# Performance work log

Measured on AMD Instinct MI355X. Metric: run time of the kernel, lower is better.

The kernel has to match this reference:

```python
import jax, jax.numpy as jnp
import numpy as np

N = 100000   # nodes
E = 1600000  # edges
D_IN = 128
D = 128
G = 64       # graphs in batch
C = 2        # out_channels
EPS = 1e-5   # BatchNorm eps


def setup_inputs() -> dict:
    key = jax.random.key(0)
    ks = jax.random.split(key, 24)
    s = 0.05
    inp = {
        "x": jax.random.normal(ks[0], (N, D_IN), dtype=jnp.float32),
        "edge_index": jax.random.randint(ks[1], (2, E), 0, N, dtype=jnp.int32),
        "edge_attr": jax.random.uniform(ks[2], (E, 2), dtype=jnp.float32),
        "batch": jnp.sort(jax.random.randint(ks[3], (N,), 0, G, dtype=jnp.int32)),
        # GCN layer 0
        "Wg0": jax.random.normal(ks[4], (D_IN, D), dtype=jnp.float32) * s,
        "bg0": jnp.zeros((D,), jnp.float32),
        "gamma0": jnp.ones((D,), jnp.float32),
        "beta0": jnp.zeros((D,), jnp.float32),
        # GCN layer 1
        "Wg1": jax.random.normal(ks[5], (D, D), dtype=jnp.float32) * s,
        "bg1": jnp.zeros((D,), jnp.float32),
        "gamma1": jnp.ones((D,), jnp.float32),
        "beta1": jnp.zeros((D,), jnp.float32),
        # dense head
        "Wl1": jax.random.normal(ks[6], (D, D), dtype=jnp.float32) * s,
        "bl1": jnp.zeros((D,), jnp.float32),
        "Wl2": jax.random.normal(ks[7], (D, D), dtype=jnp.float32) * s,
        "bl2": jnp.zeros((D,), jnp.float32),
        "Wc1": jax.random.normal(ks[8], (D, D), dtype=jnp.float32) * s,
        "bc1": jnp.zeros((D,), jnp.float32),
        "Wc2": jax.random.normal(ks[9], (D, C), dtype=jnp.float32) * s,
        "bc2": jnp.zeros((C,), jnp.float32),
    }
    return inp


def _gcn_conv(x, src, dst, w, W, b):
    # PyG GCNConv: h = x @ W ; add self-loops (weight 1) ; symmetric norm ; agg at dst ; + bias
    h = x @ W                                                   # [N, D]
    deg = jax.ops.segment_sum(w, dst, num_segments=N) + 1.0     # self-loop weight 1
    dinv = jnp.where(deg > 0, jax.lax.rsqrt(deg), 0.0)          # deg^{-1/2}
    norm = dinv[src] * w * dinv[dst]                            # [E]
    agg = jax.ops.segment_sum(norm[:, None] * h[src], dst, num_segments=N)
    agg = agg + (dinv * dinv)[:, None] * h                      # self-loop contribution
    return agg + b


def _bn(x, gamma, beta):
    # training-mode batch statistics over the node dimension
    m = x.mean(axis=0)
    v = x.var(axis=0)
    return (x - m) * jax.lax.rsqrt(v + EPS) * gamma + beta


def reference(x, edge_index, edge_attr, batch,
              Wg0, bg0, gamma0, beta0,
              Wg1, bg1, gamma1, beta1,
              Wl1, bl1, Wl2, bl2, Wc1, bc1, Wc2, bc2):
    src, dst = edge_index[0], edge_index[1]
    w = edge_attr[:, 1]  # which_edge_weight is None -> column 1

    h = jax.nn.relu(_gcn_conv(x, src, dst, w, Wg0, bg0))
    h = _bn(h, gamma0, beta0)                 # dropout: identity (eval)
    h = jax.nn.relu(_gcn_conv(h, src, dst, w, Wg1, bg1))
    h = _bn(h, gamma1, beta1)

    h = jax.nn.relu(h @ Wl1 + bl1)
    h = h @ Wl2 + bl2                          # node embeddings [N, D]

    counts = jax.ops.segment_sum(jnp.ones((N,), h.dtype), batch, num_segments=G)
    graph_reps = jax.ops.segment_sum(h, batch, num_segments=G) / jnp.maximum(counts, 1.0)[:, None]

    logits = jax.nn.relu(graph_reps @ Wc1 + bc1) @ Wc2 + bc2   # [G, C]
    return (h, graph_reps, logits)
```

## Files before the change

kernel.cpp:

```cpp
#include <hip/hip_runtime.h>

#define N_NODES 100000
#define N_EDGES 1600000
#define DFEAT   128
#define NGRAPH  64
#define EPSV    1e-5f
#define SCAN_BLOCKS ((N_NODES + 255) / 256)
#define DEG_SCALE 268435456.0f
#define DEG_MASK  ((1ULL << 42) - 1)
#define EDGE_BLOCKS ((N_EDGES + 511) / 512)
#define GEMM_GRID   ((N_NODES + 127) / 128)
#define MAXDEG 64
#define DEGSTRIDE 16

typedef float v4f  __attribute__((ext_vector_type(4)));
typedef short v8s  __attribute__((ext_vector_type(8)));
typedef unsigned short us4 __attribute__((ext_vector_type(4)));
typedef unsigned short us8 __attribute__((ext_vector_type(8)));

static __device__ __forceinline__ unsigned short f2bf(float f) {
    union { float f; unsigned int u; } v; v.f = f;
    unsigned int u = v.u;
    return (unsigned short)((u + 0x7FFFu + ((u >> 16) & 1u)) >> 16);
}
static __device__ __forceinline__ float bf2f(unsigned short b) {
    union { unsigned int u; float f; } v; v.u = ((unsigned int)b) << 16;
    return v.f;
}

__global__ __launch_bounds__(256) void initprep_kernel(
    unsigned long long* __restrict__ degcnt,
    float* __restrict__ stats0, float* __restrict__ stats1,
    float* __restrict__ gsum, float* __restrict__ gcntf,
    const float* __restrict__ W0, const float* __restrict__ W1,
    const float* __restrict__ W2, const float* __restrict__ W3,
    unsigned short* __restrict__ T0, unsigned short* __restrict__ T1,
    unsigned short* __restrict__ T2, unsigned short* __restrict__ T3) {
    int bid = blockIdx.x;
    int i = bid * 256 + threadIdx.x;
    if (i < N_NODES) degcnt[(size_t)i * DEGSTRIDE] = 0ULL;
    if (i < 256)  { stats0[i] = 0.f; stats1[i] = 0.f; }
    if (i < NGRAPH * DFEAT) gsum[i] = 0.f;
    if (i < NGRAPH) gcntf[i] = 0.f;
    if (bid < 256) {
        int which = bid >> 6;
        int i2 = (bid & 63) * 256 + threadIdx.x;
        const float* W = which == 0 ? W0 : which == 1 ? W1 : which == 2 ? W2 : W3;
        unsigned short* T = which == 0 ? T0 : which == 1 ? T1 : which == 2 ? T2 : T3;
        int n = i2 >> 7, k = i2 & 127;
        T[n * 128 + k] = f2bf(W[k * 128 + n]);
    }
}

__global__ __launch_bounds__(256, 4) void edgeplace_gemm0_kernel(
    const int* __restrict__ ei, const float* __restrict__ ea,
    unsigned long long* __restrict__ degcnt, int2* __restrict__ edges2,
    const float* __restrict__ X, const unsigned short* __restrict__ Wt,
    unsigned short* __restrict__ Out) {
    __shared__ unsigned short Ws[128][136];
    if (blockIdx.x < EDGE_BLOCKS) {
        int e0 = blockIdx.x * 512 + threadIdx.x;
        int e1 = e0 + 256;
        int sA = 0, dA = 0; float wA = 0.f; bool vA = e0 < N_EDGES;
        if (vA) { sA = ei[e0]; dA = ei[N_EDGES + e0]; wA = ea[2 * e0 + 1]; }
        int sB = 0, dB = 0; float wB = 0.f; bool vB = e1 < N_EDGES;
        if (vB) { sB = ei[e1]; dB = ei[N_EDGES + e1]; wB = ea[2 * e1 + 1]; }
        if (vA) {
            unsigned long long v = (1ULL << 42) | (unsigned long long)(wA * DEG_SCALE);
            unsigned long long old = atomicAdd(&degcnt[(size_t)dA * DEGSTRIDE], v);
            int rank = (int)(old >> 42);
            if (rank < MAXDEG)
                edges2[((size_t)dA << 6) + rank] = make_int2(sA, __float_as_int(wA));
        }
        if (vB) {
            unsigned long long v = (1ULL << 42) | (unsigned long long)(wB * DEG_SCALE);
            unsigned long long old = atomicAdd(&degcnt[(size_t)dB * DEGSTRIDE], v);
            int rank = (int)(old >> 42);
            if (rank < MAXDEG)
                edges2[((size_t)dB << 6) + rank] = make_int2(sB, __float_as_int(wB));
        }
        return;
    }
    const int tid = threadIdx.x;
    const int rb = (blockIdx.x - EDGE_BLOCKS) * 128;
#pragma unroll
    for (int it = 0; it < 8; ++it) {
        int flat = it * 2048 + tid * 8;
        int n = flat >> 7, k = flat & 127;
        *(us8*)&Ws[n][k] = *(const us8*)&Wt[n * 128 + k];
    }
    __syncthreads();

    const int wv = tid >> 6, lane = tid & 63;
    const int q = lane >> 4, c16 = lane & 15;
    const int rA = rb + wv * 32 + c16;
    const int rB = rA + 16;
    const size_t rAc = (size_t)(rA < N_NODES ? rA : N_NODES - 1);
    const size_t rBc = (size_t)(rB < N_NODES ? rB : N_NODES - 1);

    v4f acc[2][8];
#pragma unroll
    for (int i = 0; i < 2; ++i)
#pragma unroll
        for (int j = 0; j < 8; ++j) acc[i][j] = (v4f){0.f, 0.f, 0.f, 0.f};

#pragma unroll
    for (int ks = 0; ks < 4; ++ks) {
        const int k0 = ks * 32 + q * 8;
        float4 f0 = *(const float4*)&X[rAc * 128 + k0];
        float4 f1 = *(const float4*)&X[rAc * 128 + k0 + 4];
        float4 g0 = *(const float4*)&X[rBc * 128 + k0];
        float4 g1 = *(const float4*)&X[rBc * 128 + k0 + 4];
        us8 oa, ob;
        oa[0] = f2bf(f0.x); oa[1] = f2bf(f0.y); oa[2] = f2bf(f0.z); oa[3] = f2bf(f0.w);
        oa[4] = f2bf(f1.x); oa[5] = f2bf(f1.y); oa[6] = f2bf(f1.z); oa[7] = f2bf(f1.w);
        ob[0] = f2bf(g0.x); ob[1] = f2bf(g0.y); ob[2] = f2bf(g0.z); ob[3] = f2bf(g0.w);
        ob[4] = f2bf(g1.x); ob[5] = f2bf(g1.y); ob[6] = f2bf(g1.z); ob[7] = f2bf(g1.w);
        v8s a0 = *(v8s*)&oa, a1 = *(v8s*)&ob;
#pragma unroll
        for (int nt = 0; nt < 8; ++nt) {
            v8s b = *(const v8s*)&Ws[nt * 16 + c16][ks * 32 + q * 8];
            acc[0][nt] = __builtin_amdgcn_mfma_f32_16x16x32_bf16(a0, b, acc[0][nt], 0, 0, 0);
            acc[1][nt] = __builtin_amdgcn_mfma_f32_16x16x32_bf16(a1, b, acc[1][nt], 0, 0, 0);
        }
    }
#pragma unroll
    for (int mt = 0; mt < 2; ++mt)
#pragma unroll
        for (int nt = 0; nt < 8; ++nt)
#pragma unroll
            for (int r = 0; r < 4; ++r) {
                int row = rb + wv * 32 + mt * 16 + q * 4 + r;
                if (row >= N_NODES) continue;
                Out[(size_t)row * 128 + nt * 16 + c16] = f2bf(acc[mt][nt][r]);
            }
}

__global__ __launch_bounds__(256) void dinvcnt_kernel(
    const unsigned long long* __restrict__ degcnt, int* __restrict__ cnt,
    float* __restrict__ dinv) {
    int i = blockIdx.x * 256 + threadIdx.x;
    if (i >= N_NODES) return;
    unsigned long long u = degcnt[(size_t)i * DEGSTRIDE];
    int c = (int)(u >> 42);
    cnt[i] = c > MAXDEG ? MAXDEG : c;
    float deg = 1.0f + (float)(u & DEG_MASK) * (1.0f / DEG_SCALE);
    dinv[i] = rsqrtf(deg);
}

__global__ __launch_bounds__(256, 4) void gemm_bf16_kernel(
    const unsigned short* __restrict__ X,
    const unsigned short* __restrict__ Wt,
    void* __restrict__ Outv, int out_is_f32,
    const float* __restrict__ bnp, const float* __restrict__ bias, int do_relu,
    const int* __restrict__ batch, float* __restrict__ gsum,
    float* __restrict__ gcntf, int do_pool) {
    __shared__ unsigned short Ws[128][136];
    const int tid = threadIdx.x;
    const int rb = blockIdx.x * 128;

#pragma unroll
    for (int it = 0; it < 8; ++it) {
        int flat = it * 2048 + tid * 8;
        int n = flat >> 7, k = flat & 127;
        *(us8*)&Ws[n][k] = *(const us8*)&Wt[n * 128 + k];
    }
    __syncthreads();

    const int wv = tid >> 6, lane = tid & 63;
    const int q = lane >> 4, c16 = lane & 15;
    const int rA = rb + wv * 32 + c16;
    const int rB = rA + 16;
    const size_t rAc = (size_t)(rA < N_NODES ? rA : N_NODES - 1);
    const size_t rBc = (size_t)(rB < N_NODES ? rB : N_NODES - 1);

    v4f acc[2][8];
#pragma unroll
    for (int i = 0; i < 2; ++i)
#pragma unroll
        for (int j = 0; j < 8; ++j) acc[i][j] = (v4f){0.f, 0.f, 0.f, 0.f};

#pragma unroll
    for (int ks = 0; ks < 4; ++ks) {
        const int k0 = ks * 32 + q * 8;
        us8 v0 = *(const us8*)&X[rAc * 128 + k0];
        us8 v1 = *(const us8*)&X[rBc * 128 + k0];
        if (bnp) {
            float4 s0 = *(const float4*)&bnp[k0];
            float4 s1 = *(const float4*)&bnp[k0 + 4];
            float4 b0 = *(const float4*)&bnp[128 + k0];
            float4 b1 = *(const float4*)&bnp[128 + k0 + 4];
            v0[0] = f2bf(bf2f(v0[0]) * s0.x + b0.x);
            v0[1] = f2bf(bf2f(v0[1]) * s0.y + b0.y);
            v0[2] = f2bf(bf2f(v0[2]) * s0.z + b0.z);
            v0[3] = f2bf(bf2f(v0[3]) * s0.w + b0.w);
            v0[4] = f2bf(bf2f(v0[4]) * s1.x + b1.x);
            v0[5] = f2bf(bf2f(v0[5]) * s1.y + b1.y);
            v0[6] = f2bf(bf2f(v0[6]) * s1.z + b1.z);
            v0[7] = f2bf(bf2f(v0[7]) * s1.w + b1.w);
            v1[0] = f2bf(bf2f(v1[0]) * s0.x + b0.x);
            v1[1] = f2bf(bf2f(v1[1]) * s0.y + b0.y);
            v1[2] = f2bf(bf2f(v1[2]) * s0.z + b0.z);
            v1[3] = f2bf(bf2f(v1[3]) * s0.w + b0.w);
            v1[4] = f2bf(bf2f(v1[4]) * s1.x + b1.x);
            v1[5] = f2bf(bf2f(v1[5]) * s1.y + b1.y);
            v1[6] = f2bf(bf2f(v1[6]) * s1.z + b1.z);
            v1[7] = f2bf(bf2f(v1[7]) * s1.w + b1.w);
        }
        v8s a0 = *(v8s*)&v0, a1 = *(v8s*)&v1;
#pragma unroll
        for (int nt = 0; nt < 8; ++nt) {
            v8s b = *(const v8s*)&Ws[nt * 16 + c16][ks * 32 + q * 8];
            acc[0][nt] = __builtin_amdgcn_mfma_f32_16x16x32_bf16(a0, b, acc[0][nt], 0, 0, 0);
            acc[1][nt] = __builtin_amdgcn_mfma_f32_16x16x32_bf16(a1, b, acc[1][nt], 0, 0, 0);
        }
    }

#pragma unroll
    for (int mt = 0; mt < 2; ++mt) {
#pragma unroll
        for (int nt = 0; nt < 8; ++nt) {
            int col = nt * 16 + c16;
            float bcol = bias ? bias[col] : 0.f;
#pragma unroll
            for (int r = 0; r < 4; ++r) {
                int row = rb + wv * 32 + mt * 16 + q * 4 + r;
                float o = acc[mt][nt][r] + bcol;
                if (do_relu) o = fmaxf(o, 0.f);
                acc[mt][nt][r] = o;
                if (row >= N_NODES) continue;
                if (out_is_f32) ((float*)Outv)[(size_t)row * 128 + col] = o;
                else ((unsigned short*)Outv)[(size_t)row * 128 + col] = f2bf(o);
            }
        }
    }

    if (do_pool) {
        __shared__ float pg[128];
        __shared__ float pcnt;
        int br[8];
#pragma unroll
        for (int mt = 0; mt < 2; ++mt)
#pragma unroll
            for (int r = 0; r < 4; ++r) {
                int row = rb + wv * 32 + mt * 16 + q * 4 + r;
                br[mt * 4 + r] = (row < N_NODES) ? batch[row] : -1;
            }
        int rlast = (rb + 127 < N_NODES) ? rb + 127 : N_NODES - 1;
        int gmin = batch[rb];
        int gmax = batch[rlast];
        for (int g = gmin; g <= gmax; ++g) {
            if (tid < 128) pg[tid] = 0.f;
            if (tid == 0) pcnt = 0.f;
            __syncthreads();
            if (wv < 2) {
                int rr = rb + tid;
                bool p = (tid < 128) && (rr < N_NODES) && (batch[rr] == g);
                unsigned long long m = __ballot(p);
                if (lane == 0 && m) atomicAdd(&pcnt, (float)__popcll(m));
            }
#pragma unroll
            for (int nt = 0; nt < 8; ++nt) {
                float s = 0.f;
#pragma unroll
                for (int mt = 0; mt < 2; ++mt)
#pragma unroll
                    for (int r = 0; r < 4; ++r)
                        if (br[mt * 4 + r] == g) s += acc[mt][nt][r];
                s += __shfl_xor(s, 16);
                s += __shfl_xor(s, 32);
                if (q == 0 && s != 0.f) atomicAdd(&pg[nt * 16 + c16], s);
            }
            __syncthreads();
            if (tid < 128 && pg[tid] != 0.f) atomicAdd(&gsum[g * 128 + tid], pg[tid]);
            if (tid == 0 && pcnt != 0.f) atomicAdd(&gcntf[g], pcnt);
            __syncthreads();
        }
    }
}

__global__ __launch_bounds__(256) void agg_relu_bf16_kernel(
    const unsigned short* __restrict__ H, const int* __restrict__ cnt,
    const int2* __restrict__ edges2,
    const float* __restrict__ dinv, const float* __restrict__ bias,
    unsigned short* __restrict__ outb, float* __restrict__ stats, int nwaves) {
    __shared__ float red[1024];
    const int tid = threadIdx.x;
    const int wv = tid >> 6;
    const int lane = tid & 63;
    const float bx = bias[2 * lane], by = bias[2 * lane + 1];
    const unsigned int* __restrict__ H4 = (const unsigned int*)H;
    unsigned int* __restrict__ O4 = (unsigned int*)outb;
    float s0 = 0.f, q0 = 0.f, s1 = 0.f, q1 = 0.f;

    for (int i = blockIdx.x * 4 + wv; i < N_NODES; i += nwaves) {
        const int deg = __builtin_amdgcn_readfirstlane(cnt[i]);
        const int beg = i << 6;
        const int end = beg + deg;
        float di = dinv[i];
        unsigned int hs = H4[(size_t)i * 64 + lane];
        float px0 = 0.f, py0 = 0.f, px1 = 0.f, py1 = 0.f;
        float px2 = 0.f, py2 = 0.f, px3 = 0.f, py3 = 0.f;
        const int last = end - 1;
        for (int j = beg; j < end; j += 8) {
            int j1 = j + 1 < end ? j + 1 : last;
            int j2 = j + 2 < end ? j + 2 : last;
            int j3 = j + 3 < end ? j + 3 : last;
            int j4 = j + 4 < end ? j + 4 : last;
            int j5 = j + 5 < end ? j + 5 : last;
            int j6 = j + 6 < end ? j + 6 : last;
            int j7 = j + 7 < end ? j + 7 : last;
            int2 e0 = edges2[j];
            int2 e1 = edges2[j1];
            int2 e2 = edges2[j2];
            int2 e3 = edges2[j3];
            int2 e4 = edges2[j4];
            int2 e5 = edges2[j5];
            int2 e6 = edges2[j6];
            int2 e7 = edges2[j7];
            float ds0 = dinv[e0.x];
            float ds1 = dinv[e1.x];
            float ds2 = dinv[e2.x];
            float ds3 = dinv[e3.x];
            float ds4 = dinv[e4.x];
            float ds5 = dinv[e5.x];
            float ds6 = dinv[e6.x];
            float ds7 = dinv[e7.x];
            unsigned int h0 = H4[(size_t)e0.x * 64 + lane];
            unsigned int h1 = H4[(size_t)e1.x * 64 + lane];
            unsigned int h2 = H4[(size_t)e2.x * 64 + lane];
            unsigned int h3 = H4[(size_t)e3.x * 64 + lane];
            unsigned int h4 = H4[(size_t)e4.x * 64 + lane];
            unsigned int h5 = H4[(size_t)e5.x * 64 + lane];
            unsigned int h6 = H4[(size_t)e6.x * 64 + lane];
            unsigned int h7 = H4[(size_t)e7.x * 64 + lane];
            float v0 = __int_as_float(e0.y) * ds0;
            float v1 = j + 1 < end ? __int_as_float(e1.y) * ds1 : 0.f;
            float v2 = j + 2 < end ? __int_as_float(e2.y) * ds2 : 0.f;
            float v3 = j + 3 < end ? __int_as_float(e3.y) * ds3 : 0.f;
            float v4 = j + 4 < end ? __int_as_float(e4.y) * ds4 : 0.f;
            float v5 = j + 5 < end ? __int_as_float(e5.y) * ds5 : 0.f;
            float v6 = j + 6 < end ? __int_as_float(e6.y) * ds6 : 0.f;
            float v7 = j + 7 < end ? __int_as_float(e7.y) * ds7 : 0.f;
            px0 = fmaf(v0, bf2f((unsigned short)h0), px0);
            py0 = fmaf(v0, bf2f((unsigned short)(h0 >> 16)), py0);
            px1 = fmaf(v1, bf2f((unsigned short)h1), px1);
            py1 = fmaf(v1, bf2f((unsigned short)(h1 >> 16)), py1);
            px2 = fmaf(v2, bf2f((unsigned short)h2), px2);
            py2 = fmaf(v2, bf2f((unsigned short)(h2 >> 16)), py2);
            px3 = fmaf(v3, bf2f((unsigned short)h3), px3);
            py3 = fmaf(v3, bf2f((unsigned short)(h3 >> 16)), py3);
            px0 = fmaf(v4, bf2f((unsigned short)h4), px0);
            py0 = fmaf(v4, bf2f((unsigned short)(h4 >> 16)), py0);
            px1 = fmaf(v5, bf2f((unsigned short)h5), px1);
            py1 = fmaf(v5, bf2f((unsigned short)(h5 >> 16)), py1);
            px2 = fmaf(v6, bf2f((unsigned short)h6), px2);
            py2 = fmaf(v6, bf2f((unsigned short)(h6 >> 16)), py2);
            px3 = fmaf(v7, bf2f((unsigned short)h7), px3);
            py3 = fmaf(v7, bf2f((unsigned short)(h7 >> 16)), py3);
        }
        float dd = di * di;
        float ax = ((px0 + px1) + (px2 + px3)) * di;
        float ay = ((py0 + py1) + (py2 + py3)) * di;
        ax = fmaf(dd, bf2f((unsigned short)hs), ax) + bx;
        ay = fmaf(dd, bf2f((unsigned short)(hs >> 16)), ay) + by;
        ax = fmaxf(ax, 0.f);
        ay = fmaxf(ay, 0.f);
        O4[(size_t)i * 64 + lane] =
            (unsigned int)f2bf(ax) | ((unsigned int)f2bf(ay) << 16);
        s0 += ax; q0 += ax * ax; s1 += ay; q1 += ay * ay;
    }

    red[wv * 128 + 2 * lane]           = s0;
    red[wv * 128 + 2 * lane + 1]       = s1;
    red[512 + wv * 128 + 2 * lane]     = q0;
    red[512 + wv * 128 + 2 * lane + 1] = q1;
    __syncthreads();
    if (tid < 128) {
        float ts = red[tid] + red[128 + tid] + red[256 + tid] + red[384 + tid];
        float tq = red[512 + tid] + red[640 + tid] + red[768 + tid] + red[896 + tid];
        atomicAdd(&stats[tid], ts);
        atomicAdd(&stats[128 + tid], tq);
    }
}

__global__ void bn_finalize_kernel(const float* __restrict__ stats,
                                   const float* __restrict__ gamma,
                                   const float* __restrict__ beta,
                                   float* __restrict__ bnp) {
    int f = threadIdx.x;
    float mean = stats[f] / (float)N_NODES;
    float var = stats[128 + f] / (float)N_NODES - mean * mean;
    float sc = gamma[f] * rsqrtf(var + EPSV);
    bnp[f] = sc;
    bnp[128 + f] = beta[f] - mean * sc;
}

__global__ __launch_bounds__(128) void logits_kernel(
    const float* __restrict__ gsum, const float* __restrict__ gcntf,
    const float* __restrict__ Wc1, const float* __restrict__ bc1,
    const float* __restrict__ Wc2, const float* __restrict__ bc2,
    float* __restrict__ out_reps, float* __restrict__ out_logits) {
    __shared__ float repS[128];
    __shared__ float tmp[128];
    int g = blockIdx.x, t = threadIdx.x;
    float rep = gsum[(size_t)g * 128 + t] / fmaxf(gcntf[g], 1.0f);
    out_reps[(size_t)g * 128 + t] = rep;
    repS[t] = rep;
    __syncthreads();
    float acc = bc1[t];
    for (int k = 0; k < 128; ++k) acc = fmaf(repS[k], Wc1[k * 128 + t], acc);
    tmp[t] = fmaxf(acc, 0.f);
    __syncthreads();
    if (t < 2) {
        float a = bc2[t];
        for (int k = 0; k < 128; ++k) a = fmaf(tmp[k], Wc2[k * 2 + t], a);
        out_logits[g * 2 + t] = a;
    }
}

extern "C" void kernel_launch(void* const* d_in, const int* in_sizes, int n_in,
                              void* d_out, int out_size, void* d_ws, size_t ws_size,
                              hipStream_t stream) {
    const float* x      = (const float*)d_in[0];
    const int*   ei     = (const int*)d_in[1];
    const float* ea     = (const float*)d_in[2];
    const int*   batch  = (const int*)d_in[3];
    const float* Wg0    = (const float*)d_in[4];
    const float* bg0    = (const float*)d_in[5];
    const float* gamma0 = (const float*)d_in[6];
    const float* beta0  = (const float*)d_in[7];
    const float* Wg1    = (const float*)d_in[8];
    const float* bg1    = (const float*)d_in[9];
    const float* gamma1 = (const float*)d_in[10];
    const float* beta1  = (const float*)d_in[11];
    const float* Wl1    = (const float*)d_in[12];
    const float* bl1    = (const float*)d_in[13];
    const float* Wl2    = (const float*)d_in[14];
    const float* bl2    = (const float*)d_in[15];
    const float* Wc1    = (const float*)d_in[16];
    const float* bc1    = (const float*)d_in[17];
    const float* Wc2    = (const float*)d_in[18];
    const float* bc2    = (const float*)d_in[19];

    float* out = (float*)d_out;
    char* ws = (char*)d_ws;
    size_t off = 0;
    auto alloc = [&](size_t bytes) {
        void* p = ws + off;
        off += (bytes + 15) & ~(size_t)15;
        return p;
    };
    unsigned short* bufHb = (unsigned short*)alloc(sizeof(unsigned short) * (size_t)N_NODES * 128);
    unsigned short* bufAb = (unsigned short*)alloc(sizeof(unsigned short) * (size_t)N_NODES * 128);
    int2* edges2 = (int2*)alloc(sizeof(int2) * (size_t)N_NODES * MAXDEG);
    unsigned long long* degcnt = (unsigned long long*)alloc(
        sizeof(unsigned long long) * (size_t)N_NODES * DEGSTRIDE);
    unsigned short* Wt0   = (unsigned short*)alloc(sizeof(unsigned short) * 128 * 128);
    unsigned short* Wt1   = (unsigned short*)alloc(sizeof(unsigned short) * 128 * 128);
    unsigned short* Wt2   = (unsigned short*)alloc(sizeof(unsigned short) * 128 * 128);
    unsigned short* Wt3   = (unsigned short*)alloc(sizeof(unsigned short) * 128 * 128);
    float* dinv   = (float*)alloc(sizeof(float) * N_NODES);
    int*   cnt    = (int*)alloc(sizeof(int) * N_NODES);
    float* stats0 = (float*)alloc(sizeof(float) * 256);
    float* stats1 = (float*)alloc(sizeof(float) * 256);
    float* bnp0   = (float*)alloc(sizeof(float) * 256);
    float* bnp1   = (float*)alloc(sizeof(float) * 256);
    float* gsum   = (float*)alloc(sizeof(float) * NGRAPH * 128);
    float* gcntf  = (float*)alloc(sizeof(float) * NGRAPH);

    initprep_kernel<<<SCAN_BLOCKS, 256, 0, stream>>>(degcnt, stats0, stats1,
                                                     gsum, gcntf, Wg0, Wg1, Wl1, Wl2,
                                                     Wt0, Wt1, Wt2, Wt3);
    edgeplace_gemm0_kernel<<<EDGE_BLOCKS + GEMM_GRID, 256, 0, stream>>>(
        ei, ea, degcnt, edges2, x, Wt0, bufHb);
    dinvcnt_kernel<<<SCAN_BLOCKS, 256, 0, stream>>>(degcnt, cnt, dinv);

    const int agg_blocks = 2048;
    const int agg_nwaves = agg_blocks * 4;
    agg_relu_bf16_kernel<<<agg_blocks, 256, 0, stream>>>(bufHb, cnt, edges2,
                                                         dinv, bg0, bufAb, stats0, agg_nwaves);
    bn_finalize_kernel<<<1, 128, 0, stream>>>(stats0, gamma0, beta0, bnp0);
    gemm_bf16_kernel<<<GEMM_GRID, 256, 0, stream>>>(bufAb, Wt1, bufHb, 0, bnp0,
                                                    nullptr, 0, nullptr, nullptr, nullptr, 0);
    agg_relu_bf16_kernel<<<agg_blocks, 256, 0, stream>>>(bufHb, cnt, edges2,
                                                         dinv, bg1, bufAb, stats1, agg_nwaves);
    bn_finalize_kernel<<<1, 128, 0, stream>>>(stats1, gamma1, beta1, bnp1);
    gemm_bf16_kernel<<<GEMM_GRID, 256, 0, stream>>>(bufAb, Wt2, bufHb, 0, bnp1,
                                                    bl1, 1, nullptr, nullptr, nullptr, 0);
    gemm_bf16_kernel<<<GEMM_GRID, 256, 0, stream>>>(bufHb, Wt3, out, 1, nullptr,
                                                    bl2, 0, batch, gsum, gcntf, 1);
    logits_kernel<<<NGRAPH, 128, 0, stream>>>(gsum, gcntf, Wc1, bc1, Wc2, bc2,
                                              out + (size_t)N_NODES * 128,
                                              out + (size_t)N_NODES * 128 + NGRAPH * 128);
}
```

Before: 573.1 us.

## Pack degree counter into 32-bit atomics and read GEMM0 weights directly from global

Replaces the 64-bit packed count/weight-sum atomic with a 32-bit one that keeps the rank in the top 7 bits and a fixed-point weight sum with 19 fractional bits in the low 25. The slot stride is adjusted so each counter stays 128 bytes apart. The fused edge-placement/GEMM0 kernel also drops its LDS weight staging and barrier, so the MFMA B operands are loaded straight from global (L1/L2-cached) memory. This lowers atomic width and LDS use, which may raise occupancy, but loses precision in the degree sum and makes the B loads uncoalesced global reads.

```diff
diff --git a/kernel.cpp b/kernel.cpp
--- a/kernel.cpp
+++ b/kernel.cpp
@@ -6,12 +6,12 @@
 #define NGRAPH  64
 #define EPSV    1e-5f
 #define SCAN_BLOCKS ((N_NODES + 255) / 256)
-#define DEG_SCALE 268435456.0f
-#define DEG_MASK  ((1ULL << 42) - 1)
+#define W_SCALE 524288.0f
+#define W_MASK  ((1u << 25) - 1)
 #define EDGE_BLOCKS ((N_EDGES + 511) / 512)
 #define GEMM_GRID   ((N_NODES + 127) / 128)
 #define MAXDEG 64
-#define DEGSTRIDE 16
+#define DEGSTRIDE 32
 
 typedef float v4f  __attribute__((ext_vector_type(4)));
 typedef short v8s  __attribute__((ext_vector_type(8)));
@@ -29,7 +29,7 @@
 }
 
 __global__ __launch_bounds__(256) void initprep_kernel(
-    unsigned long long* __restrict__ degcnt,
+    unsigned int* __restrict__ degw,
     float* __restrict__ stats0, float* __restrict__ stats1,
     float* __restrict__ gsum, float* __restrict__ gcntf,
     const float* __restrict__ W0, const float* __restrict__ W1,
@@ -38,7 +38,7 @@
     unsigned short* __restrict__ T2, unsigned short* __restrict__ T3) {
     int bid = blockIdx.x;
     int i = bid * 256 + threadIdx.x;
-    if (i < N_NODES) degcnt[(size_t)i * DEGSTRIDE] = 0ULL;
+    if (i < N_NODES) degw[(size_t)i * DEGSTRIDE] = 0u;
     if (i < 256)  { stats0[i] = 0.f; stats1[i] = 0.f; }
     if (i < NGRAPH * DFEAT) gsum[i] = 0.f;
     if (i < NGRAPH) gcntf[i] = 0.f;
@@ -54,10 +54,9 @@
 
 __global__ __launch_bounds__(256, 4) void edgeplace_gemm0_kernel(
     const int* __restrict__ ei, const float* __restrict__ ea,
-    unsigned long long* __restrict__ degcnt, int2* __restrict__ edges2,
+    unsigned int* __restrict__ degw, int2* __restrict__ edges2,
     const float* __restrict__ X, const unsigned short* __restrict__ Wt,
     unsigned short* __restrict__ Out) {
-    __shared__ unsigned short Ws[128][136];
     if (blockIdx.x < EDGE_BLOCKS) {
         int e0 = blockIdx.x * 512 + threadIdx.x;
         int e1 = e0 + 256;
@@ -66,16 +65,16 @@
         int sB = 0, dB = 0; float wB = 0.f; bool vB = e1 < N_EDGES;
         if (vB) { sB = ei[e1]; dB = ei[N_EDGES + e1]; wB = ea[2 * e1 + 1]; }
         if (vA) {
-            unsigned long long v = (1ULL << 42) | (unsigned long long)(wA * DEG_SCALE);
-            unsigned long long old = atomicAdd(&degcnt[(size_t)dA * DEGSTRIDE], v);
-            int rank = (int)(old >> 42);
+            unsigned int v = (1u << 25) | (unsigned int)(wA * W_SCALE);
+            unsigned int old = atomicAdd(&degw[(size_t)dA * DEGSTRIDE], v);
+            int rank = (int)(old >> 25);
             if (rank < MAXDEG)
                 edges2[((size_t)dA << 6) + rank] = make_int2(sA, __float_as_int(wA));
         }
         if (vB) {
-            unsigned long long v = (1ULL << 42) | (unsigned long long)(wB * DEG_SCALE);
-            unsigned long long old = atomicAdd(&degcnt[(size_t)dB * DEGSTRIDE], v);
-            int rank = (int)(old >> 42);
+            unsigned int v = (1u << 25) | (unsigned int)(wB * W_SCALE);
+            unsigned int old = atomicAdd(&degw[(size_t)dB * DEGSTRIDE], v);
+            int rank = (int)(old >> 25);
             if (rank < MAXDEG)
                 edges2[((size_t)dB << 6) + rank] = make_int2(sB, __float_as_int(wB));
         }
@@ -83,14 +82,6 @@
     }
     const int tid = threadIdx.x;
     const int rb = (blockIdx.x - EDGE_BLOCKS) * 128;
-#pragma unroll
-    for (int it = 0; it < 8; ++it) {
-        int flat = it * 2048 + tid * 8;
-        int n = flat >> 7, k = flat & 127;
-        *(us8*)&Ws[n][k] = *(const us8*)&Wt[n * 128 + k];
-    }
-    __syncthreads();
-
     const int wv = tid >> 6, lane = tid & 63;
     const int q = lane >> 4, c16 = lane & 15;
     const int rA = rb + wv * 32 + c16;
@@ -119,7 +110,7 @@
         v8s a0 = *(v8s*)&oa, a1 = *(v8s*)&ob;
 #pragma unroll
         for (int nt = 0; nt < 8; ++nt) {
-            v8s b = *(const v8s*)&Ws[nt * 16 + c16][ks * 32 + q * 8];
+            v8s b = *(const v8s*)&Wt[(size_t)(nt * 16 + c16) * 128 + k0];
             acc[0][nt] = __builtin_amdgcn_mfma_f32_16x16x32_bf16(a0, b, acc[0][nt], 0, 0, 0);
             acc[1][nt] = __builtin_amdgcn_mfma_f32_16x16x32_bf16(a1, b, acc[1][nt], 0, 0, 0);
         }
@@ -137,14 +128,14 @@
 }
 
 __global__ __launch_bounds__(256) void dinvcnt_kernel(
-    const unsigned long long* __restrict__ degcnt, int* __restrict__ cnt,
+    const unsigned int* __restrict__ degw, int* __restrict__ cnt,
     float* __restrict__ dinv) {
     int i = blockIdx.x * 256 + threadIdx.x;
     if (i >= N_NODES) return;
-    unsigned long long u = degcnt[(size_t)i * DEGSTRIDE];
-    int c = (int)(u >> 42);
+    unsigned int u = degw[(size_t)i * DEGSTRIDE];
+    int c = (int)(u >> 25);
     cnt[i] = c > MAXDEG ? MAXDEG : c;
-    float deg = 1.0f + (float)(u & DEG_MASK) * (1.0f / DEG_SCALE);
+    float deg = 1.0f + (float)(u & W_MASK) * (1.0f / W_SCALE);
     dinv[i] = rsqrtf(deg);
 }
 
@@ -454,8 +445,8 @@
     unsigned short* bufHb = (unsigned short*)alloc(sizeof(unsigned short) * (size_t)N_NODES * 128);
     unsigned short* bufAb = (unsigned short*)alloc(sizeof(unsigned short) * (size_t)N_NODES * 128);
     int2* edges2 = (int2*)alloc(sizeof(int2) * (size_t)N_NODES * MAXDEG);
-    unsigned long long* degcnt = (unsigned long long*)alloc(
-        sizeof(unsigned long long) * (size_t)N_NODES * DEGSTRIDE);
+    unsigned int* degw = (unsigned int*)alloc(
+        sizeof(unsigned int) * (size_t)N_NODES * DEGSTRIDE);
     unsigned short* Wt0   = (unsigned short*)alloc(sizeof(unsigned short) * 128 * 128);
     unsigned short* Wt1   = (unsigned short*)alloc(sizeof(unsigned short) * 128 * 128);
     unsigned short* Wt2   = (unsigned short*)alloc(sizeof(unsigned short) * 128 * 128);
@@ -469,12 +460,12 @@
     float* gsum   = (float*)alloc(sizeof(float) * NGRAPH * 128);
     float* gcntf  = (float*)alloc(sizeof(float) * NGRAPH);
 
-    initprep_kernel<<<SCAN_BLOCKS, 256, 0, stream>>>(degcnt, stats0, stats1,
+    initprep_kernel<<<SCAN_BLOCKS, 256, 0, stream>>>(degw, stats0, stats1,
                                                      gsum, gcntf, Wg0, Wg1, Wl1, Wl2,
                                                      Wt0, Wt1, Wt2, Wt3);
     edgeplace_gemm0_kernel<<<EDGE_BLOCKS + GEMM_GRID, 256, 0, stream>>>(
-        ei, ea, degcnt, edges2, x, Wt0, bufHb);
-    dinvcnt_kernel<<<SCAN_BLOCKS, 256, 0, stream>>>(degcnt, cnt, dinv);
+        ei, ea, degw, edges2, x, Wt0, bufHb);
+    dinvcnt_kernel<<<SCAN_BLOCKS, 256, 0, stream>>>(degw, cnt, dinv);
 
     const int agg_blocks = 2048;
     const int agg_nwaves = agg_blocks * 4;
```

New measurement: 579.4 us. About the same (+1.1%).
